# Kernel tuning notes

Hardware: AMD Instinct MI355X
Metric: run time of the kernel (lower is better)

The kernel has to match this reference:

```python
import jax, jax.numpy as jnp
import numpy as np
import math

DIM = 384; HEADS = 12; HD = 32; L_REL = 4; L_STD = 12; MLP_H = 4 * DIM
B = 8; N = 256
N_REL = 1
TIME_SCALE = 30000.0 / 500 * 0.3
SCALE = HD ** -0.5
NEG = -1e9  # finite stand-in for -inf padding mask (identical softmax result, safe grads)


def _ln(x, g, b):
    m = x.mean(-1, keepdims=True)
    v = ((x - m) ** 2).mean(-1, keepdims=True)
    return (x - m) / jnp.sqrt(v + 1e-5) * g + b


def _sin_emb(x, dim):
    half = dim // 2
    freq = jnp.exp(jnp.arange(half, dtype=x.dtype) * (-math.log(10000.0) / half))
    e = x[..., None] * freq
    return jnp.concatenate([jnp.sin(e), jnp.cos(e)], -1)


def _rel_bias(x0, w1d, b1d, wp, bp):
    pos = x0[..., :3]
    t = x0[..., 3:4]
    dpos = pos[:, :, None] - pos[:, None, :]                 # [B,N,N,3]
    dt = t[:, :, None] - t[:, None, :] * TIME_SCALE          # [B,N,N,1] (scale on 2nd term, as in torch)
    dpos2 = dpos ** 2
    dt2 = dt ** 2
    ds2 = dpos2.sum(-1) - dt2[..., 0]
    d = jnp.sign(ds2) * jnp.sqrt(jnp.abs(ds2))
    f = jnp.concatenate([dpos, dt, dpos2, dt2], -1)          # [B,N,N,8]
    d = d + (f @ w1d.T + b1d)[..., 0]
    emb = _sin_emb(1024.0 * jnp.clip(d, -4.0, 4.0), HD)      # [B,N,N,HD]
    return emb @ wp.T + bp


def _mask_bias(mask):
    mn = jnp.minimum(mask[:, None, :], mask[:, :, None])
    mx = jnp.maximum(mask[:, None, :], mask[:, :, None])
    return jnp.where(mx < 0, 0.0, mn)                        # [B,N,N]


def _attn(xq, xkv, wq, wk, wv, wo, bo, rel, mbias):
    Bq, Nq, _ = xq.shape
    q = (xq @ wq.T).reshape(Bq, Nq, HEADS, HD).transpose(0, 2, 1, 3) * SCALE
    k = (xkv @ wk.T).reshape(Bq, Nq, HEADS, HD).transpose(0, 2, 1, 3)
    v = (xkv @ wv.T).reshape(Bq, Nq, HEADS, HD).transpose(0, 2, 1, 3)
    a = jnp.einsum('bhic,bhjc->bhij', q, k)
    if rel is not None:
        a = a + jnp.einsum('bhic,bijc->bhij', q, rel)
    if mbias is not None:
        a = a + mbias[:, None]
    a = jax.nn.softmax(a, axis=-1)
    o = jnp.einsum('bhij,bhjc->bihc', a, v)
    if rel is not None:
        o = o + jnp.einsum('bhij,bijc->bihc', a, rel)
    return o.reshape(Bq, Nq, HEADS * HD) @ wo.T + bo


def _mlp(x, w1, b1, w2, b2):
    return jax.nn.gelu(x @ w1.T + b1, approximate=False) @ w2.T + b2


def setup_inputs() -> dict:
    key = jax.random.key(0)
    ks = iter(jax.random.split(key, 64))
    f = lambda shape: jax.random.normal(next(ks), shape, jnp.float32) * 0.02
    inp = {}
    inp['x'] = jax.random.normal(next(ks), (B, N, DIM), jnp.float32)
    inp['x0'] = jax.random.normal(next(ks), (B, N, 4), jnp.float32)
    lengths = jax.random.randint(next(ks), (B,), N // 2, N + 1)
    inp['mask'] = jnp.where(jnp.arange(N)[None, :] < lengths[:, None], 0.0, NEG).astype(jnp.float32)
    inp['rp_w1d'] = f((1, 8)); inp['rp_b1d'] = jnp.zeros((1,), jnp.float32)
    inp['rp_wp'] = f((HD, HD)); inp['rp_bp'] = jnp.zeros((HD,), jnp.float32)
    for p, L in (('sw', L_REL), ('bl', L_STD)):
        inp[p + '_ln1_g'] = jnp.ones((L, DIM), jnp.float32); inp[p + '_ln1_b'] = jnp.zeros((L, DIM), jnp.float32)
        inp[p + '_ln2_g'] = jnp.ones((L, DIM), jnp.float32); inp[p + '_ln2_b'] = jnp.zeros((L, DIM), jnp.float32)
        inp[p + '_wq'] = f((L, DIM, DIM)); inp[p + '_wk'] = f((L, DIM, DIM)); inp[p + '_wv'] = f((L, DIM, DIM))
        inp[p + '_wo'] = f((L, DIM, DIM)); inp[p + '_bo'] = jnp.zeros((L, DIM), jnp.float32)
        inp[p + '_w1'] = f((L, MLP_H, DIM)); inp[p + '_b1'] = jnp.zeros((L, MLP_H), jnp.float32)
        inp[p + '_w2'] = f((L, DIM, MLP_H)); inp[p + '_b2'] = jnp.zeros((L, DIM), jnp.float32)
    inp['bl_g1'] = jnp.ones((L_STD, DIM), jnp.float32)   # init_values=1
    inp['bl_g2'] = jnp.ones((L_STD, DIM), jnp.float32)
    inp['cls_w'] = f((DIM,))
    inp['out_w'] = f((3, DIM)); inp['out_b'] = jnp.zeros((3,), jnp.float32)
    return inp


def reference(x, x0, mask, rp_w1d, rp_b1d, rp_wp, rp_bp,
              sw_ln1_g, sw_ln1_b, sw_ln2_g, sw_ln2_b, sw_wq, sw_wk, sw_wv, sw_wo, sw_bo,
              sw_w1, sw_b1, sw_w2, sw_b2,
              bl_ln1_g, bl_ln1_b, bl_ln2_g, bl_ln2_b, bl_wq, bl_wk, bl_wv, bl_wo, bl_bo,
              bl_w1, bl_b1, bl_w2, bl_b2, bl_g1, bl_g2, cls_w, out_w, out_b):
    rel = _rel_bias(x0, rp_w1d, rp_b1d, rp_wp, rp_bp)
    mbias = _mask_bias(mask)
    for i in range(L_REL):
        r = rel if i < N_REL else None
        xn = _ln(x, sw_ln1_g[i], sw_ln1_b[i])
        x = x + _attn(xn, xn, sw_wq[i], sw_wk[i], sw_wv[i], sw_wo[i], sw_bo[i], r, mbias)
        x = x + _mlp(_ln(x, sw_ln2_g[i], sw_ln2_b[i]), sw_w1[i], sw_b1[i], sw_w2[i], sw_b2[i])
    # prepend cls token; it is always valid
    cls = jnp.broadcast_to(cls_w[None, None, :], (x.shape[0], 1, DIM))
    x = jnp.concatenate([cls, x], axis=1)
    mask2 = jnp.concatenate([jnp.zeros((x.shape[0], 1), mask.dtype), mask], axis=1)
    mbias2 = _mask_bias(mask2)
    for i in range(L_STD):
        xn = _ln(x, bl_ln1_g[i], bl_ln1_b[i])
        x = x + bl_g1[i] * _attn(xn, xn, bl_wq[i], bl_wk[i], bl_wv[i], bl_wo[i], bl_bo[i], None, mbias2)
        x = x + bl_g2[i] * _mlp(_ln(x, bl_ln2_g[i], bl_ln2_b[i]), bl_w1[i], bl_b1[i], bl_w2[i], bl_b2[i])
    return x[:, 0] @ out_w.T + out_b   # [B, 3]
```

## Files before the change

kernel.cpp:

```cpp
#include <hip/hip_runtime.h>
#include <hip/hip_bf16.h>
#include <math.h>

#define DIM 384
#define HEADS 12
#define HD 32
#define MLP_H 1536
#define BATCH 8
#define N1 256
#define N2 257
#define QP 1152
#define SCALE 0.17677669529663687f
#define TIME_SCALE 18.0f

typedef __attribute__((ext_vector_type(8))) short frag8;
typedef __attribute__((ext_vector_type(4))) float f32x4;

__device__ inline short f2bf(float x) {
    __hip_bfloat16 h = __float2bfloat16(x);
    short s;
    __builtin_memcpy(&s, &h, 2);
    return s;
}
__device__ inline float bf2f(short s) {
    unsigned u = ((unsigned)(unsigned short)s) << 16;
    float f;
    __builtin_memcpy(&f, &u, 4);
    return f;
}

__global__ __launch_bounds__(256) void conv_kernel(
        const float* __restrict__ in, short* __restrict__ out, int n) {
    int i = (blockIdx.x * 256 + threadIdx.x) * 4;
    if (i >= n) return;
    float4 v = *(const float4*)(in + i);
    out[i]     = f2bf(v.x);
    out[i + 1] = f2bf(v.y);
    out[i + 2] = f2bf(v.z);
    out[i + 3] = f2bf(v.w);
}

__global__ __launch_bounds__(256) void conv_qkv_kernel(
        const float* __restrict__ wq, const float* __restrict__ wk,
        const float* __restrict__ wv, short* __restrict__ out, int L) {
    size_t idx = ((size_t)blockIdx.x * 256 + threadIdx.x) * 4;
    size_t total = (size_t)L * QP * DIM;
    if (idx >= total) return;
    size_t k = idx % DIM;
    size_t row = idx / DIM;
    size_t r = row % QP;
    size_t l = row / QP;
    int which = (int)(r / DIM);
    int rr = (int)(r % DIM);
    const float* src = ((which == 0) ? wq : (which == 1) ? wk : wv)
                     + (l * DIM + rr) * DIM + k;
    float4 v = *(const float4*)src;
    out[idx]     = f2bf(v.x);
    out[idx + 1] = f2bf(v.y);
    out[idx + 2] = f2bf(v.z);
    out[idx + 3] = f2bf(v.w);
}

__global__ __launch_bounds__(256) void rel_kernel(
        const float* __restrict__ x0, const float* __restrict__ w1d,
        const float* __restrict__ b1d, const float* __restrict__ wp,
        const float* __restrict__ bp, short* __restrict__ rel) {
    __shared__ float swp[HD * HD];
    __shared__ float sbp[HD];
    __shared__ float sw1[8];
    __shared__ float sb1;
    __shared__ float sfreq[16];
    int tid = threadIdx.x;
    for (int i = tid; i < HD * HD; i += 256) swp[i] = wp[i];
    if (tid < HD) sbp[tid] = bp[tid];
    if (tid < 8) sw1[tid] = w1d[tid];
    if (tid == 0) sb1 = b1d[0];
    if (tid < 16) sfreq[tid] = expf(-(float)tid * 0.5756462732485114f);
    __syncthreads();

    int gid = blockIdx.x * 256 + tid;
    int j  = gid & (N1 - 1);
    int bi = gid >> 8;
    int i  = bi & (N1 - 1);
    int b  = bi >> 8;

    const float* pi = x0 + (size_t)(b * N1 + i) * 4;
    const float* pj = x0 + (size_t)(b * N1 + j) * 4;
    float dx = pi[0] - pj[0], dy = pi[1] - pj[1], dz = pi[2] - pj[2];
    float dt = pi[3] - pj[3] * TIME_SCALE;
    float dx2 = dx * dx, dy2 = dy * dy, dz2 = dz * dz, dt2 = dt * dt;
    float ds2 = dx2 + dy2 + dz2 - dt2;
    float d = copysignf(sqrtf(fabsf(ds2)), ds2);
    d += dx * sw1[0] + dy * sw1[1] + dz * sw1[2] + dt * sw1[3]
       + dx2 * sw1[4] + dy2 * sw1[5] + dz2 * sw1[6] + dt2 * sw1[7] + sb1;
    d = fminf(fmaxf(d, -4.f), 4.f) * 1024.f;

    float emb[32];
    #pragma unroll
    for (int k = 0; k < 16; k++) {
        float s, c;
        sincosf(d * sfreq[k], &s, &c);
        emb[k] = s; emb[16 + k] = c;
    }
    short* out = rel + (size_t)gid * HD;
    #pragma unroll 4
    for (int c = 0; c < HD; c++) {
        float a = sbp[c];
        #pragma unroll
        for (int k = 0; k < 32; k++) a += emb[k] * swp[c * 32 + k];
        out[c] = f2bf(a);
    }
}

__global__ __launch_bounds__(256) void rel_score_kernel(
        const short* __restrict__ qkv, const short* __restrict__ relb,
        short* __restrict__ rs) {
    int tid = threadIdx.x;
    int w = tid >> 6, lane = tid & 63;
    int n = lane & 15, quad = lane >> 4;
    int i = blockIdx.x * 4 + w;
    int b = blockIdx.y;

    const frag8 fz = {0, 0, 0, 0, 0, 0, 0, 0};
    frag8 qa = fz;
    if (n < HEADS)
        qa = *(const frag8*)(qkv + ((size_t)(b * N1) + i) * QP + n * HD + quad * 8);

    const short* relrow = relb + (((size_t)(b * N1) + i) * N1) * HD;
    const f32x4 z = {0.f, 0.f, 0.f, 0.f};

    #pragma unroll 4
    for (int jt = 0; jt < 16; jt++) {
        frag8 rb = *(const frag8*)(relrow + (size_t)(jt * 16 + n) * HD + quad * 8);
        f32x4 s = __builtin_amdgcn_mfma_f32_16x16x32_bf16(qa, rb, z, 0, 0, 0);
        #pragma unroll
        for (int r = 0; r < 4; r++) {
            int h = quad * 4 + r;
            if (h < HEADS)
                rs[((size_t)(b * HEADS + h) * N1 + i) * N1 + jt * 16 + n] =
                    f2bf(s[r] * SCALE);
        }
    }
}

__global__ __launch_bounds__(256) void rel_pv_kernel(
        const short* __restrict__ pglob, const short* __restrict__ relb,
        const float* __restrict__ omain, short* __restrict__ ob) {
    __shared__ short vt[4][2][2][64][8];
    int tid = threadIdx.x;
    int w = tid >> 6, lane = tid & 63;
    int n = lane & 15, quad = lane >> 4;
    int i = blockIdx.x * 4 + w;
    int b = blockIdx.y;
    size_t rowB = (size_t)(b * N1);

    const frag8 fz = {0, 0, 0, 0, 0, 0, 0, 0};
    f32x4 oa0 = {0.f, 0.f, 0.f, 0.f}, oa1 = {0.f, 0.f, 0.f, 0.f};
    const short* relrow = relb + ((rowB + i) * (size_t)N1) * HD;
    const short* prow = pglob + ((size_t)(b * HEADS + (n < HEADS ? n : 0)) * N1 + i) * N1;
    bool hval = (n < HEADS);

    int jr = lane & 31;
    int cb = (lane >> 5) * 16;

    #pragma unroll 2
    for (int kk = 0; kk < 8; kk++) {
        int par = kk & 1;
        const short* rr = relrow + (size_t)(kk * 32 + jr) * HD + cb;
        frag8 rv0 = *(const frag8*)rr;
        frag8 rv1 = *(const frag8*)(rr + 8);
        #pragma unroll
        for (int e = 0; e < 8; e++) {
            int c0 = cb + e, c1 = cb + 8 + e;
            vt[w][par][c0 >> 4][(jr >> 3) * 16 + (c0 & 15)][jr & 7] = rv0[e];
            vt[w][par][c1 >> 4][(jr >> 3) * 16 + (c1 & 15)][jr & 7] = rv1[e];
        }
        frag8 pa = fz;
        if (hval) pa = *(const frag8*)(prow + kk * 32 + quad * 8);
        frag8 b0 = *(const frag8*)&vt[w][par][0][lane][0];
        frag8 b1 = *(const frag8*)&vt[w][par][1][lane][0];
        oa0 = __builtin_amdgcn_mfma_f32_16x16x32_bf16(pa, b0, oa0, 0, 0, 0);
        oa1 = __builtin_amdgcn_mfma_f32_16x16x32_bf16(pa, b1, oa1, 0, 0, 0);
    }

    #pragma unroll
    for (int r = 0; r < 4; r++) {
        int h = quad * 4 + r;
        if (h < HEADS) {
            size_t o0 = (rowB + i) * DIM + h * HD + n;
            ob[o0]      = f2bf(omain[o0]      + oa0[r]);
            ob[o0 + 16] = f2bf(omain[o0 + 16] + oa1[r]);
        }
    }
}

__global__ __launch_bounds__(128) void ln_kernel(
        const float* __restrict__ x, const float* __restrict__ g,
        const float* __restrict__ b, short* __restrict__ y) {
    int r = blockIdx.x;
    int t = threadIdx.x;
    const float* xr = x + (size_t)r * DIM;
    float v0 = xr[t], v1 = xr[t + 128], v2 = xr[t + 256];
    __shared__ float redm[2], redv[2];
    float s = v0 + v1 + v2;
    for (int o = 32; o; o >>= 1) s += __shfl_down(s, o, 64);
    int lane = t & 63, wid = t >> 6;
    if (!lane) redm[wid] = s;
    __syncthreads();
    float mean = (redm[0] + redm[1]) * (1.f / DIM);
    float d0 = v0 - mean, d1 = v1 - mean, d2 = v2 - mean;
    float s2 = d0 * d0 + d1 * d1 + d2 * d2;
    for (int o = 32; o; o >>= 1) s2 += __shfl_down(s2, o, 64);
    if (!lane) redv[wid] = s2;
    __syncthreads();
    float var = (redv[0] + redv[1]) * (1.f / DIM);
    float rs = rsqrtf(var + 1e-5f);
    short* yr = y + (size_t)r * DIM;
    yr[t]       = f2bf(d0 * rs * g[t]       + b[t]);
    yr[t + 128] = f2bf(d1 * rs * g[t + 128] + b[t + 128]);
    yr[t + 256] = f2bf(d2 * rs * g[t + 256] + b[t + 256]);
}

__global__ __launch_bounds__(512) void gemm_bf16_kernel(
        const short* __restrict__ A, const short* __restrict__ W,
        const float* __restrict__ bias, const float* __restrict__ resid,
        const float* __restrict__ gvec, float* __restrict__ Cf,
        short* __restrict__ Cb, int M, int Np, int K, int mode) {
    __shared__ short As2[2][2][4][64][8];
    __shared__ short Bs2[2][2][4][64][8];
    int tid = threadIdx.x;
    int w = tid >> 6, lane = tid & 63;
    int nlo = lane & 15, quad = lane >> 4;
    int g = w >> 2, wl = w & 3;
    int wm = wl >> 1, wn = wl & 1;
    int n0 = blockIdx.x * 64, m0 = blockIdx.y * 64;

    f32x4 acc00 = {0.f, 0.f, 0.f, 0.f}, acc01 = {0.f, 0.f, 0.f, 0.f};
    f32x4 acc10 = {0.f, 0.f, 0.f, 0.f}, acc11 = {0.f, 0.f, 0.f, 0.f};

    int oct16 = tid & 15, rbase = tid >> 4;
    int kh_s = oct16 >> 3, oo = oct16 & 7, ks_s = oo >> 2, q_s = oo & 3;
    const frag8 fz = {0, 0, 0, 0, 0, 0, 0, 0};
    frag8 pa0 = fz, pa1 = fz, pb0, pb1;

    {
        int gm0 = m0 + rbase, gm1 = m0 + rbase + 32;
        if (gm0 < M) pa0 = *(const frag8*)(A + (size_t)gm0 * K + oct16 * 8);
        if (gm1 < M) pa1 = *(const frag8*)(A + (size_t)gm1 * K + oct16 * 8);
        pb0 = *(const frag8*)(W + (size_t)(n0 + rbase) * K + oct16 * 8);
        pb1 = *(const frag8*)(W + (size_t)(n0 + rbase + 32) * K + oct16 * 8);
    }

    for (int k0 = 0; k0 < K; k0 += 128) {
        *(frag8*)&As2[kh_s][ks_s][q_s][rbase][0]      = pa0;
        *(frag8*)&As2[kh_s][ks_s][q_s][rbase + 32][0] = pa1;
        *(frag8*)&Bs2[kh_s][ks_s][q_s][rbase][0]      = pb0;
        *(frag8*)&Bs2[kh_s][ks_s][q_s][rbase + 32][0] = pb1;
        __syncthreads();
        int kn = k0 + 128;
        if (kn < K) {
            int gm0 = m0 + rbase, gm1 = m0 + rbase + 32;
            pa0 = fz; pa1 = fz;
            if (gm0 < M) pa0 = *(const frag8*)(A + (size_t)gm0 * K + kn + oct16 * 8);
            if (gm1 < M) pa1 = *(const frag8*)(A + (size_t)gm1 * K + kn + oct16 * 8);
            pb0 = *(const frag8*)(W + (size_t)(n0 + rbase) * K + kn + oct16 * 8);
            pb1 = *(const frag8*)(W + (size_t)(n0 + rbase + 32) * K + kn + oct16 * 8);
        }
        #pragma unroll
        for (int ks = 0; ks < 2; ks++) {
            frag8 a0 = *(const frag8*)&As2[g][ks][quad][wm * 32 + nlo][0];
            frag8 a1 = *(const frag8*)&As2[g][ks][quad][wm * 32 + 16 + nlo][0];
            frag8 b0 = *(const frag8*)&Bs2[g][ks][quad][wn * 32 + nlo][0];
            frag8 b1 = *(const frag8*)&Bs2[g][ks][quad][wn * 32 + 16 + nlo][0];
            acc00 = __builtin_amdgcn_mfma_f32_16x16x32_bf16(a0, b0, acc00, 0, 0, 0);
            acc01 = __builtin_amdgcn_mfma_f32_16x16x32_bf16(a0, b1, acc01, 0, 0, 0);
            acc10 = __builtin_amdgcn_mfma_f32_16x16x32_bf16(a1, b0, acc10, 0, 0, 0);
            acc11 = __builtin_amdgcn_mfma_f32_16x16x32_bf16(a1, b1, acc11, 0, 0, 0);
        }
        __syncthreads();
    }

    f32x4* red4 = (f32x4*)&As2[0][0][0][0][0];
    int roff = wl * 64 + lane;
    if (g == 1) {
        red4[roff]       = acc00;
        red4[256 + roff] = acc01;
        red4[512 + roff] = acc10;
        red4[768 + roff] = acc11;
    }
    __syncthreads();
    if (g == 1) return;
    {
        f32x4 t0 = red4[roff], t1 = red4[256 + roff];
        f32x4 t2 = red4[512 + roff], t3 = red4[768 + roff];
        #pragma unroll
        for (int r = 0; r < 4; r++) {
            acc00[r] += t0[r]; acc01[r] += t1[r];
            acc10[r] += t2[r]; acc11[r] += t3[r];
        }
    }

    #pragma unroll
    for (int mi = 0; mi < 2; mi++) {
        #pragma unroll
        for (int nf = 0; nf < 2; nf++) {
            f32x4 av = (mi == 0) ? ((nf == 0) ? acc00 : acc01)
                                 : ((nf == 0) ? acc10 : acc11);
            int col = n0 + wn * 32 + nf * 16 + nlo;
            float bcol = (mode >= 1) ? bias[col] : 0.f;
            float gs = 1.f;
            if (mode == 2 && gvec) gs = gvec[col];
            #pragma unroll
            for (int r = 0; r < 4; r++) {
                int row = m0 + wm * 32 + mi * 16 + quad * 4 + r;
                if (row >= M) continue;
                float v = av[r] + bcol;
                if (mode == 1) v = 0.5f * v * (1.f + erff(v * 0.70710678118654752f));
                if (mode == 2) {
                    Cf[(size_t)row * Np + col] = resid[(size_t)row * Np + col] + gs * v;
                } else {
                    Cb[(size_t)row * Np + col] = f2bf(v);
                }
            }
        }
    }
}

__global__ __launch_bounds__(256) void attn_mfma_kernel(
        const short* __restrict__ qkv, const float* __restrict__ maskv,
        short* __restrict__ ob, int Nseq) {
    __shared__ short kf[18][64][8];
    __shared__ short vf[9][2][64][8];
    __shared__ short pbuf[4][2][16][40];
    __shared__ float ms[320];

    int tid = threadIdx.x;
    int w = tid >> 6, lane = tid & 63;
    int n = lane & 15, quad = lane >> 4;
    int qg = blockIdx.x, h = blockIdx.y, b = blockIdx.z;
    size_t rowB = (size_t)(b * Nseq);

    for (int j = tid; j < 320; j += 256)
        ms[j] = (j < Nseq) ? maskv[b * Nseq + j] : 0.f;

    {
        int c0 = (tid & 3) * 8;
        for (int j = tid >> 2; j < 288; j += 64) {
            frag8 kk = {0, 0, 0, 0, 0, 0, 0, 0};
            frag8 vv = {0, 0, 0, 0, 0, 0, 0, 0};
            if (j < Nseq) {
                const short* base = qkv + (rowB + j) * QP + h * HD + c0;
                kk = *(const frag8*)(base + 384);
                vv = *(const frag8*)(base + 768);
            }
            *(frag8*)&kf[j >> 4][(c0 >> 3) * 16 + (j & 15)][0] = kk;
            #pragma unroll
            for (int e = 0; e < 8; e++) {
                int c = c0 + e;
                vf[j >> 5][c >> 4][((j & 31) >> 3) * 16 + (c & 15)][j & 7] = vv[e];
            }
        }
    }

    int i0 = qg * 64 + w * 16;
    frag8 qa = {0, 0, 0, 0, 0, 0, 0, 0};
    {
        int i = i0 + n;
        if (i < Nseq) qa = *(const frag8*)(qkv + (rowB + i) * QP + h * HD + quad * 8);
    }
    __syncthreads();

    float msq[4];
    #pragma unroll
    for (int r = 0; r < 4; r++) msq[r] = ms[i0 + quad * 4 + r];

    float mrow[4], lsum[4];
    #pragma unroll
    for (int r = 0; r < 4; r++) { mrow[r] = -3.0e38f; lsum[r] = 0.f; }
    f32x4 oacc0 = {0.f, 0.f, 0.f, 0.f}, oacc1 = {0.f, 0.f, 0.f, 0.f};

    for (int jb = 0; jb < 9; jb++) {
        int par = jb & 1;
        frag8 kb0 = *(const frag8*)&kf[2 * jb][lane][0];
        frag8 kb1 = *(const frag8*)&kf[2 * jb + 1][lane][0];
        f32x4 z = {0.f, 0.f, 0.f, 0.f};
        f32x4 s0 = __builtin_amdgcn_mfma_f32_16x16x32_bf16(qa, kb0, z, 0, 0, 0);
        f32x4 s1 = __builtin_amdgcn_mfma_f32_16x16x32_bf16(qa, kb1, z, 0, 0, 0);

        int j0 = jb * 32 + n;
        int j1 = j0 + 16;
        float mj0 = ms[j0], mj1 = ms[j1];
        float pad0 = (j0 < Nseq) ? 0.f : -1e9f;
        float pad1 = (j1 < Nseq) ? 0.f : -1e9f;

        #pragma unroll
        for (int r = 0; r < 4; r++) {
            float mi = msq[r];
            float b0 = ((fmaxf(mi, mj0) < 0.f) ? 0.f : fminf(mi, mj0)) + pad0;
            float b1 = ((fmaxf(mi, mj1) < 0.f) ? 0.f : fminf(mi, mj1)) + pad1;
            float v0 = s0[r] * SCALE + b0;
            float v1 = s1[r] * SCALE + b1;
            float rm = fmaxf(v0, v1);
            rm = fmaxf(rm, __shfl_xor(rm, 1));
            rm = fmaxf(rm, __shfl_xor(rm, 2));
            rm = fmaxf(rm, __shfl_xor(rm, 4));
            rm = fmaxf(rm, __shfl_xor(rm, 8));
            float mn = fmaxf(mrow[r], rm);
            float alpha = __expf(mrow[r] - mn);
            mrow[r] = mn;
            float p0 = __expf(v0 - mn);
            float p1 = __expf(v1 - mn);
            float ps = p0 + p1;
            ps += __shfl_xor(ps, 1);
            ps += __shfl_xor(ps, 2);
            ps += __shfl_xor(ps, 4);
            ps += __shfl_xor(ps, 8);
            lsum[r] = lsum[r] * alpha + ps;
            oacc0[r] *= alpha;
            oacc1[r] *= alpha;
            pbuf[w][par][quad * 4 + r][n]      = f2bf(p0);
            pbuf[w][par][quad * 4 + r][n + 16] = f2bf(p1);
        }
        frag8 pa = *(const frag8*)&pbuf[w][par][n][quad * 8];
        frag8 vb0 = *(const frag8*)&vf[jb][0][lane][0];
        frag8 vb1 = *(const frag8*)&vf[jb][1][lane][0];
        oacc0 = __builtin_amdgcn_mfma_f32_16x16x32_bf16(pa, vb0, oacc0, 0, 0, 0);
        oacc1 = __builtin_amdgcn_mfma_f32_16x16x32_bf16(pa, vb1, oacc1, 0, 0, 0);
    }

    #pragma unroll
    for (int r = 0; r < 4; r++) {
        int i = i0 + quad * 4 + r;
        if (i < Nseq) {
            float invl = 1.f / lsum[r];
            ob[(rowB + i) * DIM + h * HD + n]      = f2bf(oacc0[r] * invl);
            ob[(rowB + i) * DIM + h * HD + 16 + n] = f2bf(oacc1[r] * invl);
        }
    }
}

__global__ __launch_bounds__(128) void attn_rel_mfma_kernel(
        const short* __restrict__ qkv, short* __restrict__ rs,
        const float* __restrict__ maskv, float* __restrict__ omain) {
    const int Nseq = N1;
    __shared__ short kf[16][64][8];
    __shared__ short vf[8][2][64][8];
    __shared__ short pbuf[2][2][16][40];
    __shared__ float ms[256];

    int tid = threadIdx.x;
    int w = tid >> 6, lane = tid & 63;
    int n = lane & 15, quad = lane >> 4;
    int qg = blockIdx.x, h = blockIdx.y, b = blockIdx.z;
    size_t rowB = (size_t)(b * Nseq);

    for (int jj = tid; jj < 256; jj += 128) ms[jj] = maskv[b * Nseq + jj];

    {
        int c0 = (tid & 3) * 8;
        for (int j = tid >> 2; j < 256; j += 32) {
            const short* base = qkv + (rowB + j) * QP + h * HD + c0;
            frag8 kk = *(const frag8*)(base + 384);
            frag8 vv = *(const frag8*)(base + 768);
            *(frag8*)&kf[j >> 4][(c0 >> 3) * 16 + (j & 15)][0] = kk;
            #pragma unroll
            for (int e = 0; e < 8; e++) {
                int c = c0 + e;
                vf[j >> 5][c >> 4][((j & 31) >> 3) * 16 + (c & 15)][j & 7] = vv[e];
            }
        }
    }

    int i0 = qg * 32 + w * 16;
    frag8 qa = *(const frag8*)(qkv + (rowB + i0 + n) * QP + h * HD + quad * 8);
    __syncthreads();

    float msq[4];
    short* rsp[4];
    #pragma unroll
    for (int r = 0; r < 4; r++) {
        msq[r] = ms[i0 + quad * 4 + r];
        rsp[r] = rs + ((size_t)(b * HEADS + h) * N1 + (i0 + quad * 4 + r)) * N1;
    }

    float sv0[32], sv1[32];
    float rmax[4];
    #pragma unroll
    for (int r = 0; r < 4; r++) rmax[r] = -3.0e38f;

    #pragma unroll
    for (int jb = 0; jb < 8; jb++) {
        frag8 kb0 = *(const frag8*)&kf[2 * jb][lane][0];
        frag8 kb1 = *(const frag8*)&kf[2 * jb + 1][lane][0];
        f32x4 z = {0.f, 0.f, 0.f, 0.f};
        f32x4 s0 = __builtin_amdgcn_mfma_f32_16x16x32_bf16(qa, kb0, z, 0, 0, 0);
        f32x4 s1 = __builtin_amdgcn_mfma_f32_16x16x32_bf16(qa, kb1, z, 0, 0, 0);
        int j0 = jb * 32 + n;
        int j1 = j0 + 16;
        float mj0 = ms[j0], mj1 = ms[j1];
        #pragma unroll
        for (int r = 0; r < 4; r++) {
            float d0 = bf2f(rsp[r][j0]);
            float d1 = bf2f(rsp[r][j1]);
            float mi = msq[r];
            float b0 = (fmaxf(mi, mj0) < 0.f) ? 0.f : fminf(mi, mj0);
            float b1 = (fmaxf(mi, mj1) < 0.f) ? 0.f : fminf(mi, mj1);
            float v0 = s0[r] * SCALE + d0 + b0;
            float v1 = s1[r] * SCALE + d1 + b1;
            sv0[jb * 4 + r] = v0;
            sv1[jb * 4 + r] = v1;
            rmax[r] = fmaxf(rmax[r], fmaxf(v0, v1));
        }
    }
    #pragma unroll
    for (int r = 0; r < 4; r++) {
        float rm = rmax[r];
        rm = fmaxf(rm, __shfl_xor(rm, 1));
        rm = fmaxf(rm, __shfl_xor(rm, 2));
        rm = fmaxf(rm, __shfl_xor(rm, 4));
        rm = fmaxf(rm, __shfl_xor(rm, 8));
        rmax[r] = rm;
    }

    float lsum[4] = {0.f, 0.f, 0.f, 0.f};
    #pragma unroll
    for (int jb = 0; jb < 8; jb++) {
        #pragma unroll
        for (int r = 0; r < 4; r++) {
            float p0 = __expf(sv0[jb * 4 + r] - rmax[r]);
            float p1 = __expf(sv1[jb * 4 + r] - rmax[r]);
            sv0[jb * 4 + r] = p0;
            sv1[jb * 4 + r] = p1;
            lsum[r] += p0 + p1;
        }
    }
    float invl[4];
    #pragma unroll
    for (int r = 0; r < 4; r++) {
        float ls = lsum[r];
        ls += __shfl_xor(ls, 1);
        ls += __shfl_xor(ls, 2);
        ls += __shfl_xor(ls, 4);
        ls += __shfl_xor(ls, 8);
        invl[r] = 1.f / ls;
    }

    f32x4 oacc0 = {0.f, 0.f, 0.f, 0.f}, oacc1 = {0.f, 0.f, 0.f, 0.f};
    #pragma unroll
    for (int jb = 0; jb < 8; jb++) {
        int par = jb & 1;
        #pragma unroll
        for (int r = 0; r < 4; r++) {
            short h0 = f2bf(sv0[jb * 4 + r] * invl[r]);
            short h1 = f2bf(sv1[jb * 4 + r] * invl[r]);
            pbuf[w][par][quad * 4 + r][n]      = h0;
            pbuf[w][par][quad * 4 + r][n + 16] = h1;
            rsp[r][jb * 32 + n]      = h0;
            rsp[r][jb * 32 + n + 16] = h1;
        }
        frag8 pa = *(const frag8*)&pbuf[w][par][n][quad * 8];
        frag8 vb0 = *(const frag8*)&vf[jb][0][lane][0];
        frag8 vb1 = *(const frag8*)&vf[jb][1][lane][0];
        oacc0 = __builtin_amdgcn_mfma_f32_16x16x32_bf16(pa, vb0, oacc0, 0, 0, 0);
        oacc1 = __builtin_amdgcn_mfma_f32_16x16x32_bf16(pa, vb1, oacc1, 0, 0, 0);
    }

    #pragma unroll
    for (int r = 0; r < 4; r++) {
        int i = i0 + quad * 4 + r;
        omain[(rowB + i) * DIM + h * HD + n]      = oacc0[r];
        omain[(rowB + i) * DIM + h * HD + 16 + n] = oacc1[r];
    }
}

__global__ __launch_bounds__(256) void concat_kernel(
        const float* __restrict__ xa, const float* __restrict__ clsw,
        const float* __restrict__ mask, float* __restrict__ xb,
        float* __restrict__ m2) {
    int idx = blockIdx.x * 256 + threadIdx.x;
    const int total = BATCH * N2 * DIM;
    if (idx < total) {
        int c = idx % DIM;
        int tokb = idx / DIM;
        int p = tokb % N2, b = tokb / N2;
        xb[idx] = (p == 0) ? clsw[c] : xa[((size_t)(b * N1) + p - 1) * DIM + c];
    }
    if (idx < BATCH * N2) {
        int p = idx % N2, b = idx / N2;
        m2[idx] = (p == 0) ? 0.f : mask[b * N1 + p - 1];
    }
}

__global__ __launch_bounds__(64) void head_kernel(
        const float* __restrict__ xb, const float* __restrict__ ow,
        const float* __restrict__ obv, float* __restrict__ out) {
    int blk = blockIdx.x;
    int b = blk / 3, o = blk % 3;
    int lane = threadIdx.x;
    const float* xr = xb + (size_t)(b * N2) * DIM;
    const float* wr = ow + o * DIM;
    float s = 0.f;
    for (int c = lane; c < DIM; c += 64) s += xr[c] * wr[c];
    for (int off = 32; off; off >>= 1) s += __shfl_down(s, off, 64);
    if (!lane) out[blk] = s + obv[o];
}

extern "C" void kernel_launch(void* const* d_in, const int* in_sizes, int n_in,
                              void* d_out, int out_size, void* d_ws, size_t ws_size,
                              hipStream_t stream) {
    (void)in_sizes; (void)n_in; (void)out_size; (void)ws_size;
    const float* X       = (const float*)d_in[0];
    const float* X0      = (const float*)d_in[1];
    const float* MSK     = (const float*)d_in[2];
    const float* RW1     = (const float*)d_in[3];
    const float* RB1     = (const float*)d_in[4];
    const float* RWP     = (const float*)d_in[5];
    const float* RBP     = (const float*)d_in[6];
    const float* SW_LN1G = (const float*)d_in[7];
    const float* SW_LN1B = (const float*)d_in[8];
    const float* SW_LN2G = (const float*)d_in[9];
    const float* SW_LN2B = (const float*)d_in[10];
    const float* SW_WQ   = (const float*)d_in[11];
    const float* SW_WK   = (const float*)d_in[12];
    const float* SW_WV   = (const float*)d_in[13];
    const float* SW_WO   = (const float*)d_in[14];
    const float* SW_BO   = (const float*)d_in[15];
    const float* SW_W1   = (const float*)d_in[16];
    const float* SW_B1   = (const float*)d_in[17];
    const float* SW_W2   = (const float*)d_in[18];
    const float* SW_B2   = (const float*)d_in[19];
    const float* BL_LN1G = (const float*)d_in[20];
    const float* BL_LN1B = (const float*)d_in[21];
    const float* BL_LN2G = (const float*)d_in[22];
    const float* BL_LN2B = (const float*)d_in[23];
    const float* BL_WQ   = (const float*)d_in[24];
    const float* BL_WK   = (const float*)d_in[25];
    const float* BL_WV   = (const float*)d_in[26];
    const float* BL_WO   = (const float*)d_in[27];
    const float* BL_BO   = (const float*)d_in[28];
    const float* BL_W1   = (const float*)d_in[29];
    const float* BL_B1   = (const float*)d_in[30];
    const float* BL_W2   = (const float*)d_in[31];
    const float* BL_B2   = (const float*)d_in[32];
    const float* BL_G1   = (const float*)d_in[33];
    const float* BL_G2   = (const float*)d_in[34];
    const float* CLSW    = (const float*)d_in[35];
    const float* OUTW    = (const float*)d_in[36];
    const float* OUTB    = (const float*)d_in[37];

    const int T1 = BATCH * N1;
    const int T2 = BATCH * N2;
    const size_t RELSZ = (size_t)BATCH * N1 * N1 * HD;

    short* rel = (short*)d_ws;
    float* xa  = (float*)(rel + RELSZ);
    float* xb  = xa + (size_t)T1 * DIM;
    float* m2  = xb + (size_t)T2 * DIM;
    short* sbase = (short*)(m2 + 2064);
    short* xn   = sbase;
    short* qkv  = xn  + (size_t)T2 * DIM;
    short* ab   = qkv + (size_t)T2 * QP;
    short* hb   = ab  + (size_t)T2 * DIM;
    short* cw_qkv_sw = hb + (size_t)T2 * MLP_H;
    short* cw_qkv_bl = cw_qkv_sw + (size_t)4  * QP * DIM;
    short* cw_wo_sw  = cw_qkv_bl + (size_t)12 * QP * DIM;
    short* cw_wo_bl  = cw_wo_sw  + (size_t)4  * DIM * DIM;
    short* cw_w1_sw  = cw_wo_bl  + (size_t)12 * DIM * DIM;
    short* cw_w1_bl  = cw_w1_sw  + (size_t)4  * MLP_H * DIM;
    short* cw_w2_sw  = cw_w1_bl  + (size_t)12 * MLP_H * DIM;
    short* cw_w2_bl  = cw_w2_sw  + (size_t)4  * DIM * MLP_H;
    short* rs_buf    = cw_w2_bl  + (size_t)12 * DIM * MLP_H;
    float* omain     = (float*)hb;

    conv_qkv_kernel<<<(4 * QP * DIM / 4 + 255) / 256, 256, 0, stream>>>(SW_WQ, SW_WK, SW_WV, cw_qkv_sw, 4);
    conv_qkv_kernel<<<(12 * QP * DIM / 4 + 255) / 256, 256, 0, stream>>>(BL_WQ, BL_WK, BL_WV, cw_qkv_bl, 12);
    conv_kernel<<<(4 * DIM * DIM / 4 + 255) / 256, 256, 0, stream>>>(SW_WO, cw_wo_sw, 4 * DIM * DIM);
    conv_kernel<<<(12 * DIM * DIM / 4 + 255) / 256, 256, 0, stream>>>(BL_WO, cw_wo_bl, 12 * DIM * DIM);
    conv_kernel<<<(4 * MLP_H * DIM / 4 + 255) / 256, 256, 0, stream>>>(SW_W1, cw_w1_sw, 4 * MLP_H * DIM);
    conv_kernel<<<(12 * MLP_H * DIM / 4 + 255) / 256, 256, 0, stream>>>(BL_W1, cw_w1_bl, 12 * MLP_H * DIM);
    conv_kernel<<<(4 * DIM * MLP_H / 4 + 255) / 256, 256, 0, stream>>>(SW_W2, cw_w2_sw, 4 * DIM * MLP_H);
    conv_kernel<<<(12 * DIM * MLP_H / 4 + 255) / 256, 256, 0, stream>>>(BL_W2, cw_w2_bl, 12 * DIM * MLP_H);

    rel_kernel<<<BATCH * N1 * N1 / 256, 256, 0, stream>>>(X0, RW1, RB1, RWP, RBP, rel);
    hipMemcpyAsync(xa, X, sizeof(float) * T1 * DIM, hipMemcpyDeviceToDevice, stream);

    dim3 gQ1(QP / 64, T1 / 64);
    dim3 gP1(DIM / 64, T1 / 64);
    dim3 gM1(MLP_H / 64, T1 / 64);
    dim3 gF1(4, HEADS, BATCH);
    dim3 gRel(8, HEADS, BATCH);
    for (int l = 0; l < 4; l++) {
        const short* wqkv = cw_qkv_sw + (size_t)l * QP * DIM;
        const short* wo = cw_wo_sw + (size_t)l * DIM * DIM;
        const short* w1 = cw_w1_sw + (size_t)l * MLP_H * DIM;
        const short* w2 = cw_w2_sw + (size_t)l * DIM * MLP_H;
        const float* bo = SW_BO + (size_t)l * DIM;
        const float* b1 = SW_B1 + (size_t)l * MLP_H;
        const float* b2 = SW_B2 + (size_t)l * DIM;

        ln_kernel<<<T1, 128, 0, stream>>>(xa, SW_LN1G + l * DIM, SW_LN1B + l * DIM, xn);
        gemm_bf16_kernel<<<gQ1, 512, 0, stream>>>(xn, wqkv, nullptr, nullptr, nullptr,
                                                  nullptr, qkv, T1, QP, DIM, 0);
        if (l == 0) {
            rel_score_kernel<<<dim3(N1 / 4, BATCH), 256, 0, stream>>>(qkv, rel, rs_buf);
            attn_rel_mfma_kernel<<<gRel, 128, 0, stream>>>(qkv, rs_buf, MSK, omain);
            rel_pv_kernel<<<dim3(N1 / 4, BATCH), 256, 0, stream>>>(rs_buf, rel, omain, ab);
        } else {
            attn_mfma_kernel<<<gF1, 256, 0, stream>>>(qkv, MSK, ab, N1);
        }
        gemm_bf16_kernel<<<gP1, 512, 0, stream>>>(ab, wo, bo, xa, nullptr,
                                                  xa, nullptr, T1, DIM, DIM, 2);
        ln_kernel<<<T1, 128, 0, stream>>>(xa, SW_LN2G + l * DIM, SW_LN2B + l * DIM, xn);
        gemm_bf16_kernel<<<gM1, 512, 0, stream>>>(xn, w1, b1, nullptr, nullptr,
                                                  nullptr, hb, T1, MLP_H, DIM, 1);
        gemm_bf16_kernel<<<gP1, 512, 0, stream>>>(hb, w2, b2, xa, nullptr,
                                                  xa, nullptr, T1, DIM, MLP_H, 2);
    }

    concat_kernel<<<(BATCH * N2 * DIM + 255) / 256, 256, 0, stream>>>(xa, CLSW, MSK, xb, m2);

    int MB2 = (T2 + 63) / 64;
    dim3 gQ2(QP / 64, MB2);
    dim3 gP2(DIM / 64, MB2);
    dim3 gM2(MLP_H / 64, MB2);
    dim3 gF2(5, HEADS, BATCH);
    for (int l = 0; l < 12; l++) {
        const short* wqkv = cw_qkv_bl + (size_t)l * QP * DIM;
        const short* wo = cw_wo_bl + (size_t)l * DIM * DIM;
        const short* w1 = cw_w1_bl + (size_t)l * MLP_H * DIM;
        const short* w2 = cw_w2_bl + (size_t)l * DIM * MLP_H;
        const float* bo = BL_BO + (size_t)l * DIM;
        const float* b1 = BL_B1 + (size_t)l * MLP_H;
        const float* b2 = BL_B2 + (size_t)l * DIM;
        const float* g1 = BL_G1 + (size_t)l * DIM;
        const float* g2 = BL_G2 + (size_t)l * DIM;

        ln_kernel<<<T2, 128, 0, stream>>>(xb, BL_LN1G + l * DIM, BL_LN1B + l * DIM, xn);
        gemm_bf16_kernel<<<gQ2, 512, 0, stream>>>(xn, wqkv, nullptr, nullptr, nullptr,
                                                  nullptr, qkv, T2, QP, DIM, 0);
        attn_mfma_kernel<<<gF2, 256, 0, stream>>>(qkv, m2, ab, N2);
        gemm_bf16_kernel<<<gP2, 512, 0, stream>>>(ab, wo, bo, xb, g1,
                                                  xb, nullptr, T2, DIM, DIM, 2);
        ln_kernel<<<T2, 128, 0, stream>>>(xb, BL_LN2G + l * DIM, BL_LN2B + l * DIM, xn);
        gemm_bf16_kernel<<<gM2, 512, 0, stream>>>(xn, w1, b1, nullptr, nullptr,
                                                  nullptr, hb, T2, MLP_H, DIM, 1);
        gemm_bf16_kernel<<<gP2, 512, 0, stream>>>(hb, w2, b2, xb, g2,
                                                  xb, nullptr, T2, DIM, MLP_H, 2);
    }

    head_kernel<<<BATCH * 3, 64, 0, stream>>>(xb, OUTW, OUTB, (float*)d_out);
}
```

Measured before the change: 1.755 ms.

## Fuse LayerNorm into QKV/MLP-up GEMMs and use MFMA for rel-bias projection

```diff
diff --git a/kernel.cpp b/kernel.cpp
--- a/kernel.cpp
+++ b/kernel.cpp
@@ -65,20 +65,27 @@
         const float* __restrict__ x0, const float* __restrict__ w1d,
         const float* __restrict__ b1d, const float* __restrict__ wp,
         const float* __restrict__ bp, short* __restrict__ rel) {
-    __shared__ float swp[HD * HD];
-    __shared__ float sbp[HD];
     __shared__ float sw1[8];
-    __shared__ float sb1;
-    __shared__ float sfreq[16];
+    __shared__ float sb1s[1];
+    __shared__ short scr[4][64][40];
     int tid = threadIdx.x;
-    for (int i = tid; i < HD * HD; i += 256) swp[i] = wp[i];
-    if (tid < HD) sbp[tid] = bp[tid];
+    int w = tid >> 6, lane = tid & 63;
+    int n = lane & 15, quad = lane >> 4;
     if (tid < 8) sw1[tid] = w1d[tid];
-    if (tid == 0) sb1 = b1d[0];
-    if (tid < 16) sfreq[tid] = expf(-(float)tid * 0.5756462732485114f);
+    if (tid == 0) sb1s[0] = b1d[0];
+
+    frag8 wb0, wb1;
+    #pragma unroll
+    for (int e = 0; e < 8; e++) {
+        wb0[e] = f2bf(wp[n * 32 + quad * 8 + e]);
+        wb1[e] = f2bf(wp[(n + 16) * 32 + quad * 8 + e]);
+    }
+    float bp0 = bp[n], bp1 = bp[n + 16];
     __syncthreads();
-
-    int gid = blockIdx.x * 256 + tid;
+    float sb1 = sb1s[0];
+
+    int gbase = blockIdx.x * 256 + w * 64;
+    int gid = gbase + lane;
     int j  = gid & (N1 - 1);
     int bi = gid >> 8;
     int i  = bi & (N1 - 1);
@@ -95,20 +102,39 @@
        + dx2 * sw1[4] + dy2 * sw1[5] + dz2 * sw1[6] + dt2 * sw1[7] + sb1;
     d = fminf(fmaxf(d, -4.f), 4.f) * 1024.f;
 
-    float emb[32];
+    const float freq[16] = {
+        1.0f, 0.56234132519f, 0.31622776602f, 0.17782794100f,
+        0.1f, 0.056234132519f, 0.031622776602f, 0.017782794100f,
+        0.01f, 0.0056234132519f, 0.0031622776602f, 0.0017782794100f,
+        0.001f, 0.00056234132519f, 0.00031622776602f, 0.00017782794100f};
     #pragma unroll
     for (int k = 0; k < 16; k++) {
-        float s, c;
-        sincosf(d * sfreq[k], &s, &c);
-        emb[k] = s; emb[16 + k] = c;
-    }
-    short* out = rel + (size_t)gid * HD;
-    #pragma unroll 4
-    for (int c = 0; c < HD; c++) {
-        float a = sbp[c];
-        #pragma unroll
-        for (int k = 0; k < 32; k++) a += emb[k] * swp[c * 32 + k];
-        out[c] = f2bf(a);
+        float rev = d * freq[k] * 0.15915494309189535f;
+        rev = rev - floorf(rev);
+        float s = __builtin_amdgcn_sinf(rev);
+        float c = __builtin_amdgcn_cosf(rev);
+        scr[w][lane][k]      = f2bf(s);
+        scr[w][lane][16 + k] = f2bf(c);
+    }
+
+    #pragma unroll
+    for (int g16 = 0; g16 < 4; g16++) {
+        frag8 ea = *(const frag8*)&scr[w][g16 * 16 + n][quad * 8];
+        f32x4 z = {0.f, 0.f, 0.f, 0.f};
+        f32x4 s0 = __builtin_amdgcn_mfma_f32_16x16x32_bf16(ea, wb0, z, 0, 0, 0);
+        f32x4 s1 = __builtin_amdgcn_mfma_f32_16x16x32_bf16(ea, wb1, z, 0, 0, 0);
+        #pragma unroll
+        for (int r = 0; r < 4; r++) {
+            scr[w][g16 * 16 + quad * 4 + r][n]      = f2bf(s0[r] + bp0);
+            scr[w][g16 * 16 + quad * 4 + r][n + 16] = f2bf(s1[r] + bp1);
+        }
+    }
+
+    short* dst = rel + (size_t)gbase * HD;
+    #pragma unroll
+    for (int s = 0; s < 4; s++) {
+        frag8 v = *(const frag8*)&scr[w][s * 16 + (lane >> 2)][(lane & 3) * 8];
+        *(frag8*)(dst + s * 512 + lane * 8) = v;
     }
 }
 
@@ -192,33 +218,6 @@
             ob[o0 + 16] = f2bf(omain[o0 + 16] + oa1[r]);
         }
     }
-}
-
-__global__ __launch_bounds__(128) void ln_kernel(
-        const float* __restrict__ x, const float* __restrict__ g,
-        const float* __restrict__ b, short* __restrict__ y) {
-    int r = blockIdx.x;
-    int t = threadIdx.x;
-    const float* xr = x + (size_t)r * DIM;
-    float v0 = xr[t], v1 = xr[t + 128], v2 = xr[t + 256];
-    __shared__ float redm[2], redv[2];
-    float s = v0 + v1 + v2;
-    for (int o = 32; o; o >>= 1) s += __shfl_down(s, o, 64);
-    int lane = t & 63, wid = t >> 6;
-    if (!lane) redm[wid] = s;
-    __syncthreads();
-    float mean = (redm[0] + redm[1]) * (1.f / DIM);
-    float d0 = v0 - mean, d1 = v1 - mean, d2 = v2 - mean;
-    float s2 = d0 * d0 + d1 * d1 + d2 * d2;
-    for (int o = 32; o; o >>= 1) s2 += __shfl_down(s2, o, 64);
-    if (!lane) redv[wid] = s2;
-    __syncthreads();
-    float var = (redv[0] + redv[1]) * (1.f / DIM);
-    float rs = rsqrtf(var + 1e-5f);
-    short* yr = y + (size_t)r * DIM;
-    yr[t]       = f2bf(d0 * rs * g[t]       + b[t]);
-    yr[t + 128] = f2bf(d1 * rs * g[t + 128] + b[t + 128]);
-    yr[t + 256] = f2bf(d2 * rs * g[t + 256] + b[t + 256]);
 }
 
 __global__ __launch_bounds__(512) void gemm_bf16_kernel(
@@ -321,6 +320,173 @@
                 } else {
                     Cb[(size_t)row * Np + col] = f2bf(v);
                 }
+            }
+        }
+    }
+}
+
+__global__ __launch_bounds__(512) void gemm_ln_kernel(
+        const float* __restrict__ X, const float* __restrict__ lng,
+        const float* __restrict__ lnb, const short* __restrict__ W,
+        const float* __restrict__ bias, short* __restrict__ Cb,
+        int M, int Np, int mode) {
+    const int K = DIM;
+    __shared__ short As2[2][2][4][64][8];
+    __shared__ short Bs2[2][2][4][64][8];
+    __shared__ __align__(16) float sg[DIM];
+    __shared__ __align__(16) float sbv[DIM];
+    __shared__ float smean[64], srstd[64];
+
+    int tid = threadIdx.x;
+    int w = tid >> 6, lane = tid & 63;
+    int nlo = lane & 15, quad = lane >> 4;
+    int g = w >> 2, wl = w & 3;
+    int wm = wl >> 1, wn = wl & 1;
+    int n0 = blockIdx.x * 64, m0 = blockIdx.y * 64;
+
+    if (tid < DIM) { sg[tid] = lng[tid]; sbv[tid] = lnb[tid]; }
+    {
+        int rrow = tid >> 3, l8 = tid & 7;
+        float sum = 0.f, ssq = 0.f;
+        if (m0 + rrow < M) {
+            const float* xr = X + (size_t)(m0 + rrow) * K + l8 * 4;
+            #pragma unroll
+            for (int ii = 0; ii < 12; ii++) {
+                float4 v = *(const float4*)(xr + ii * 32);
+                sum += v.x + v.y + v.z + v.w;
+                ssq += v.x * v.x + v.y * v.y + v.z * v.z + v.w * v.w;
+            }
+        }
+        sum += __shfl_xor(sum, 1); ssq += __shfl_xor(ssq, 1);
+        sum += __shfl_xor(sum, 2); ssq += __shfl_xor(ssq, 2);
+        sum += __shfl_xor(sum, 4); ssq += __shfl_xor(ssq, 4);
+        if (l8 == 0) {
+            float mean = sum * (1.f / K);
+            float var = fmaxf(ssq * (1.f / K) - mean * mean, 0.f);
+            smean[rrow] = mean;
+            srstd[rrow] = rsqrtf(var + 1e-5f);
+        }
+    }
+    __syncthreads();
+
+    f32x4 acc00 = {0.f, 0.f, 0.f, 0.f}, acc01 = {0.f, 0.f, 0.f, 0.f};
+    f32x4 acc10 = {0.f, 0.f, 0.f, 0.f}, acc11 = {0.f, 0.f, 0.f, 0.f};
+
+    int oct16 = tid & 15, rbase = tid >> 4;
+    int kh_s = oct16 >> 3, oo = oct16 & 7, ks_s = oo >> 2, q_s = oo & 3;
+
+    float mA0 = smean[rbase],      rA0 = srstd[rbase];
+    float mA1 = smean[rbase + 32], rA1 = srstd[rbase + 32];
+
+    float4 zf4 = {0.f, 0.f, 0.f, 0.f};
+    float4 a0lo = zf4, a0hi = zf4, a1lo = zf4, a1hi = zf4;
+    frag8 pb0, pb1;
+    {
+        int gm0 = m0 + rbase, gm1 = m0 + rbase + 32;
+        if (gm0 < M) {
+            const float* pA = X + (size_t)gm0 * K + oct16 * 8;
+            a0lo = *(const float4*)pA; a0hi = *(const float4*)(pA + 4);
+        }
+        if (gm1 < M) {
+            const float* pA = X + (size_t)gm1 * K + oct16 * 8;
+            a1lo = *(const float4*)pA; a1hi = *(const float4*)(pA + 4);
+        }
+        pb0 = *(const frag8*)(W + (size_t)(n0 + rbase) * K + oct16 * 8);
+        pb1 = *(const frag8*)(W + (size_t)(n0 + rbase + 32) * K + oct16 * 8);
+    }
+
+    for (int k0 = 0; k0 < K; k0 += 128) {
+        int koff = k0 + oct16 * 8;
+        float4 g0 = *(const float4*)&sg[koff];
+        float4 g1 = *(const float4*)&sg[koff + 4];
+        float4 b0v = *(const float4*)&sbv[koff];
+        float4 b1v = *(const float4*)&sbv[koff + 4];
+        frag8 na0, na1;
+        na0[0] = f2bf((a0lo.x - mA0) * rA0 * g0.x + b0v.x);
+        na0[1] = f2bf((a0lo.y - mA0) * rA0 * g0.y + b0v.y);
+        na0[2] = f2bf((a0lo.z - mA0) * rA0 * g0.z + b0v.z);
+        na0[3] = f2bf((a0lo.w - mA0) * rA0 * g0.w + b0v.w);
+        na0[4] = f2bf((a0hi.x - mA0) * rA0 * g1.x + b1v.x);
+        na0[5] = f2bf((a0hi.y - mA0) * rA0 * g1.y + b1v.y);
+        na0[6] = f2bf((a0hi.z - mA0) * rA0 * g1.z + b1v.z);
+        na0[7] = f2bf((a0hi.w - mA0) * rA0 * g1.w + b1v.w);
+        na1[0] = f2bf((a1lo.x - mA1) * rA1 * g0.x + b0v.x);
+        na1[1] = f2bf((a1lo.y - mA1) * rA1 * g0.y + b0v.y);
+        na1[2] = f2bf((a1lo.z - mA1) * rA1 * g0.z + b0v.z);
+        na1[3] = f2bf((a1lo.w - mA1) * rA1 * g0.w + b0v.w);
+        na1[4] = f2bf((a1hi.x - mA1) * rA1 * g1.x + b1v.x);
+        na1[5] = f2bf((a1hi.y - mA1) * rA1 * g1.y + b1v.y);
+        na1[6] = f2bf((a1hi.z - mA1) * rA1 * g1.z + b1v.z);
+        na1[7] = f2bf((a1hi.w - mA1) * rA1 * g1.w + b1v.w);
+        *(frag8*)&As2[kh_s][ks_s][q_s][rbase][0]      = na0;
+        *(frag8*)&As2[kh_s][ks_s][q_s][rbase + 32][0] = na1;
+        *(frag8*)&Bs2[kh_s][ks_s][q_s][rbase][0]      = pb0;
+        *(frag8*)&Bs2[kh_s][ks_s][q_s][rbase + 32][0] = pb1;
+        __syncthreads();
+        int kn = k0 + 128;
+        if (kn < K) {
+            int gm0 = m0 + rbase, gm1 = m0 + rbase + 32;
+            a0lo = zf4; a0hi = zf4; a1lo = zf4; a1hi = zf4;
+            if (gm0 < M) {
+                const float* pA = X + (size_t)gm0 * K + kn + oct16 * 8;
+                a0lo = *(const float4*)pA; a0hi = *(const float4*)(pA + 4);
+            }
+            if (gm1 < M) {
+                const float* pA = X + (size_t)gm1 * K + kn + oct16 * 8;
+                a1lo = *(const float4*)pA; a1hi = *(const float4*)(pA + 4);
+            }
+            pb0 = *(const frag8*)(W + (size_t)(n0 + rbase) * K + kn + oct16 * 8);
+            pb1 = *(const frag8*)(W + (size_t)(n0 + rbase + 32) * K + kn + oct16 * 8);
+        }
+        #pragma unroll
+        for (int ks = 0; ks < 2; ks++) {
+            frag8 a0 = *(const frag8*)&As2[g][ks][quad][wm * 32 + nlo][0];
+            frag8 a1 = *(const frag8*)&As2[g][ks][quad][wm * 32 + 16 + nlo][0];
+            frag8 b0 = *(const frag8*)&Bs2[g][ks][quad][wn * 32 + nlo][0];
+            frag8 b1 = *(const frag8*)&Bs2[g][ks][quad][wn * 32 + 16 + nlo][0];
+            acc00 = __builtin_amdgcn_mfma_f32_16x16x32_bf16(a0, b0, acc00, 0, 0, 0);
+            acc01 = __builtin_amdgcn_mfma_f32_16x16x32_bf16(a0, b1, acc01, 0, 0, 0);
+            acc10 = __builtin_amdgcn_mfma_f32_16x16x32_bf16(a1, b0, acc10, 0, 0, 0);
+            acc11 = __builtin_amdgcn_mfma_f32_16x16x32_bf16(a1, b1, acc11, 0, 0, 0);
+        }
+        __syncthreads();
+    }
+
+    f32x4* red4 = (f32x4*)&As2[0][0][0][0][0];
+    int roff = wl * 64 + lane;
+    if (g == 1) {
+        red4[roff]       = acc00;
+        red4[256 + roff] = acc01;
+        red4[512 + roff] = acc10;
+        red4[768 + roff] = acc11;
+    }
+    __syncthreads();
+    if (g == 1) return;
+    {
+        f32x4 t0 = red4[roff], t1 = red4[256 + roff];
+        f32x4 t2 = red4[512 + roff], t3 = red4[768 + roff];
+        #pragma unroll
+        for (int r = 0; r < 4; r++) {
+            acc00[r] += t0[r]; acc01[r] += t1[r];
+            acc10[r] += t2[r]; acc11[r] += t3[r];
+        }
+    }
+
+    #pragma unroll
+    for (int mi = 0; mi < 2; mi++) {
+        #pragma unroll
+        for (int nf = 0; nf < 2; nf++) {
+            f32x4 av = (mi == 0) ? ((nf == 0) ? acc00 : acc01)
+                                 : ((nf == 0) ? acc10 : acc11);
+            int col = n0 + wn * 32 + nf * 16 + nlo;
+            float bcol = (mode == 1) ? bias[col] : 0.f;
+            #pragma unroll
+            for (int r = 0; r < 4; r++) {
+                int row = m0 + wm * 32 + mi * 16 + quad * 4 + r;
+                if (row >= M) continue;
+                float v = av[r] + bcol;
+                if (mode == 1) v = 0.5f * v * (1.f + erff(v * 0.70710678118654752f));
+                Cb[(size_t)row * Np + col] = f2bf(v);
             }
         }
     }
@@ -698,9 +864,8 @@
         const float* b1 = SW_B1 + (size_t)l * MLP_H;
         const float* b2 = SW_B2 + (size_t)l * DIM;
 
-        ln_kernel<<<T1, 128, 0, stream>>>(xa, SW_LN1G + l * DIM, SW_LN1B + l * DIM, xn);
-        gemm_bf16_kernel<<<gQ1, 512, 0, stream>>>(xn, wqkv, nullptr, nullptr, nullptr,
-                                                  nullptr, qkv, T1, QP, DIM, 0);
+        gemm_ln_kernel<<<gQ1, 512, 0, stream>>>(xa, SW_LN1G + l * DIM, SW_LN1B + l * DIM,
+                                                wqkv, nullptr, qkv, T1, QP, 0);
         if (l == 0) {
             rel_score_kernel<<<dim3(N1 / 4, BATCH), 256, 0, stream>>>(qkv, rel, rs_buf);
             attn_rel_mfma_kernel<<<gRel, 128, 0, stream>>>(qkv, rs_buf, MSK, omain);
@@ -710,9 +875,8 @@
         }
         gemm_bf16_kernel<<<gP1, 512, 0, stream>>>(ab, wo, bo, xa, nullptr,
                                                   xa, nullptr, T1, DIM, DIM, 2);
-        ln_kernel<<<T1, 128, 0, stream>>>(xa, SW_LN2G + l * DIM, SW_LN2B + l * DIM, xn);
-        gemm_bf16_kernel<<<gM1, 512, 0, stream>>>(xn, w1, b1, nullptr, nullptr,
-                                                  nullptr, hb, T1, MLP_H, DIM, 1);
+        gemm_ln_kernel<<<gM1, 512, 0, stream>>>(xa, SW_LN2G + l * DIM, SW_LN2B + l * DIM,
+                                                w1, b1, hb, T1, MLP_H, 1);
         gemm_bf16_kernel<<<gP1, 512, 0, stream>>>(hb, w2, b2, xa, nullptr,
                                                   xa, nullptr, T1, DIM, MLP_H, 2);
     }
@@ -735,15 +899,13 @@
         const float* g1 = BL_G1 + (size_t)l * DIM;
         const float* g2 = BL_G2 + (size_t)l * DIM;
 
-        ln_kernel<<<T2, 128, 0, stream>>>(xb, BL_LN1G + l * DIM, BL_LN1B + l * DIM, xn);
-        gemm_bf16_kernel<<<gQ2, 512, 0, stream>>>(xn, wqkv, nullptr, nullptr, nullptr,
-                                                  nullptr, qkv, T2, QP, DIM, 0);
+        gemm_ln_kernel<<<gQ2, 512, 0, stream>>>(xb, BL_LN1G + l * DIM, BL_LN1B + l * DIM,
+                                                wqkv, nullptr, qkv, T2, QP, 0);
         attn_mfma_kernel<<<gF2, 256, 0, stream>>>(qkv, m2, ab, N2);
         gemm_bf16_kernel<<<gP2, 512, 0, stream>>>(ab, wo, bo, xb, g1,
                                                   xb, nullptr, T2, DIM, DIM, 2);
-        ln_kernel<<<T2, 128, 0, stream>>>(xb, BL_LN2G + l * DIM, BL_LN2B + l * DIM, xn);
-        gemm_bf16_kernel<<<gM2, 512, 0, stream>>>(xn, w1, b1, nullptr, nullptr,
-                                                  nullptr, hb, T2, MLP_H, DIM, 1);
+        gemm_ln_kernel<<<gM2, 512, 0, stream>>>(xb, BL_LN2G + l * DIM, BL_LN2B + l * DIM,
+                                                w1, b1, hb, T2, MLP_H, 1);
         gemm_bf16_kernel<<<gP2, 512, 0, stream>>>(hb, w2, b2, xb, g2,
                                                   xb, nullptr, T2, DIM, MLP_H, 2);
     }
```

Measured after the change: 1.867 ms. 1.06x slower.

## Compute relative-position projection with MFMA and hardware sin/cos in rel_kernel

Applied to the files above, without the earlier changes.

```diff
diff --git a/kernel.cpp b/kernel.cpp
--- a/kernel.cpp
+++ b/kernel.cpp
@@ -65,20 +65,27 @@
         const float* __restrict__ x0, const float* __restrict__ w1d,
         const float* __restrict__ b1d, const float* __restrict__ wp,
         const float* __restrict__ bp, short* __restrict__ rel) {
-    __shared__ float swp[HD * HD];
-    __shared__ float sbp[HD];
     __shared__ float sw1[8];
-    __shared__ float sb1;
-    __shared__ float sfreq[16];
+    __shared__ float sb1s[1];
+    __shared__ short scr[4][64][40];
     int tid = threadIdx.x;
-    for (int i = tid; i < HD * HD; i += 256) swp[i] = wp[i];
-    if (tid < HD) sbp[tid] = bp[tid];
+    int w = tid >> 6, lane = tid & 63;
+    int n = lane & 15, quad = lane >> 4;
     if (tid < 8) sw1[tid] = w1d[tid];
-    if (tid == 0) sb1 = b1d[0];
-    if (tid < 16) sfreq[tid] = expf(-(float)tid * 0.5756462732485114f);
+    if (tid == 0) sb1s[0] = b1d[0];
+
+    frag8 wb0, wb1;
+    #pragma unroll
+    for (int e = 0; e < 8; e++) {
+        wb0[e] = f2bf(wp[n * 32 + quad * 8 + e]);
+        wb1[e] = f2bf(wp[(n + 16) * 32 + quad * 8 + e]);
+    }
+    float bp0 = bp[n], bp1 = bp[n + 16];
     __syncthreads();
-
-    int gid = blockIdx.x * 256 + tid;
+    float sb1 = sb1s[0];
+
+    int gbase = blockIdx.x * 256 + w * 64;
+    int gid = gbase + lane;
     int j  = gid & (N1 - 1);
     int bi = gid >> 8;
     int i  = bi & (N1 - 1);
@@ -95,20 +102,39 @@
        + dx2 * sw1[4] + dy2 * sw1[5] + dz2 * sw1[6] + dt2 * sw1[7] + sb1;
     d = fminf(fmaxf(d, -4.f), 4.f) * 1024.f;
 
-    float emb[32];
+    const float freq[16] = {
+        1.0f, 0.56234132519f, 0.31622776602f, 0.17782794100f,
+        0.1f, 0.056234132519f, 0.031622776602f, 0.017782794100f,
+        0.01f, 0.0056234132519f, 0.0031622776602f, 0.0017782794100f,
+        0.001f, 0.00056234132519f, 0.00031622776602f, 0.00017782794100f};
     #pragma unroll
     for (int k = 0; k < 16; k++) {
-        float s, c;
-        sincosf(d * sfreq[k], &s, &c);
-        emb[k] = s; emb[16 + k] = c;
-    }
-    short* out = rel + (size_t)gid * HD;
-    #pragma unroll 4
-    for (int c = 0; c < HD; c++) {
-        float a = sbp[c];
-        #pragma unroll
-        for (int k = 0; k < 32; k++) a += emb[k] * swp[c * 32 + k];
-        out[c] = f2bf(a);
+        float rev = d * freq[k] * 0.15915494309189535f;
+        rev = rev - floorf(rev);
+        float s = __builtin_amdgcn_sinf(rev);
+        float c = __builtin_amdgcn_cosf(rev);
+        scr[w][lane][k]      = f2bf(s);
+        scr[w][lane][16 + k] = f2bf(c);
+    }
+
+    #pragma unroll
+    for (int g16 = 0; g16 < 4; g16++) {
+        frag8 ea = *(const frag8*)&scr[w][g16 * 16 + n][quad * 8];
+        f32x4 z = {0.f, 0.f, 0.f, 0.f};
+        f32x4 s0 = __builtin_amdgcn_mfma_f32_16x16x32_bf16(ea, wb0, z, 0, 0, 0);
+        f32x4 s1 = __builtin_amdgcn_mfma_f32_16x16x32_bf16(ea, wb1, z, 0, 0, 0);
+        #pragma unroll
+        for (int r = 0; r < 4; r++) {
+            scr[w][g16 * 16 + quad * 4 + r][n]      = f2bf(s0[r] + bp0);
+            scr[w][g16 * 16 + quad * 4 + r][n + 16] = f2bf(s1[r] + bp1);
+        }
+    }
+
+    short* dst = rel + (size_t)gbase * HD;
+    #pragma unroll
+    for (int s = 0; s < 4; s++) {
+        frag8 v = *(const frag8*)&scr[w][s * 16 + (lane >> 2)][(lane & 3) * 8];
+        *(frag8*)(dst + s * 512 + lane * 8) = v;
     }
 }
 
```

New measurement: 1.728 ms. About the same (-1.5%).
